# Performance work log

Hardware: AMD Instinct MI355X
Metric: run time of the kernel (lower is better)

## Reference

```python
import jax, jax.numpy as jnp
import numpy as np
import math

CH = 256
GROUPS = max(min(CH // 4, 32), 1)  # default_num_groups -> 32
EPS = 1e-5


def group_norm(x, gamma, beta):
    # x: [B, C, H, W]
    B, C, H, W = x.shape
    xg = x.reshape(B, GROUPS, C // GROUPS, H, W)
    mu = jnp.mean(xg, axis=(2, 3, 4), keepdims=True)
    var = jnp.var(xg, axis=(2, 3, 4), keepdims=True)
    xn = ((xg - mu) * jax.lax.rsqrt(var + EPS)).reshape(B, C, H, W)
    return xn * gamma[None, :, None, None] + beta[None, :, None, None]


def conv1x1(x, w, b):
    # x: [B, C_in, H, W]; w: [C_out, C_in]; b: [C_out]
    return jnp.einsum('oc,bchw->bohw', w, x) + b[None, :, None, None]


def xavier(key, shape, gain):
    fan_in, fan_out = shape[1], shape[0]
    limit = gain * math.sqrt(6.0 / (fan_in + fan_out))
    return jax.random.uniform(key, shape, jnp.float32, -limit, limit)


def setup_inputs() -> dict:
    key = jax.random.key(0)
    ks = jax.random.split(key, 6)
    x = jax.random.normal(ks[0], (32, CH, 32, 32), jnp.float32)
    gamma = jnp.ones((CH,), jnp.float32)
    beta = jnp.zeros((CH,), jnp.float32)
    g = math.sqrt(0.1)  # init_scale=0.1 for q,k,v
    wq = xavier(ks[1], (CH, CH), g)
    wk = xavier(ks[2], (CH, CH), g)
    wv = xavier(ks[3], (CH, CH), g)
    # w_h uses init_scale=0.0 -> zeros in original; use small nonzero so output is exercised
    wh = xavier(ks[4], (CH, CH), 0.1)
    bq = jnp.zeros((CH,), jnp.float32)
    bk = jnp.zeros((CH,), jnp.float32)
    bv = jnp.zeros((CH,), jnp.float32)
    bh = jnp.zeros((CH,), jnp.float32)
    return dict(x=x, gamma=gamma, beta=beta, wq=wq, bq=bq, wk=wk, bk=bk,
                wv=wv, bv=bv, wh=wh, bh=bh)


def reference(x, gamma, beta, wq, bq, wk, bk, wv, bv, wh, bh):
    B, C, H, W = x.shape
    N = H * W
    h = group_norm(x, gamma, beta)
    q = conv1x1(h, wq, bq).reshape(B, C, N)
    k = conv1x1(h, wk, bk).reshape(B, C, N)
    v = conv1x1(h, wv, bv).reshape(B, C, N)
    # full attention over spatial tokens: scores [B, N, N]
    scores = jnp.einsum('bcn,bcm->bnm', q, k) / math.sqrt(C)
    attn = jax.nn.softmax(scores, axis=-1)
    h = jnp.einsum('bnm,bcm->bcn', attn, v).reshape(B, C, H, W)
    h = conv1x1(h, wh, bh)
    return x + h  # skip_rescale=False
```

## Files before the change

kernel.cpp:

```cpp
#include <hip/hip_runtime.h>

typedef __bf16 bf16_t;
typedef __bf16 bf16x8 __attribute__((ext_vector_type(8)));
typedef __bf16 bf16x4 __attribute__((ext_vector_type(4)));
typedef float f32x4 __attribute__((ext_vector_type(4)));
typedef float f32x16 __attribute__((ext_vector_type(16)));
typedef long longx2 __attribute__((ext_vector_type(2)));

static constexpr int kC = 256;
static constexpr int kN = 1024;
static constexpr int kB = 32;

__device__ __forceinline__ void gload_lds16(const void* g, void* l) {
  __builtin_amdgcn_global_load_lds(
      (const __attribute__((address_space(1))) unsigned int*)g,
      (__attribute__((address_space(3))) unsigned int*)l, 16, 0, 0);
}

__device__ __forceinline__ unsigned cvt_pk_bf16(float a, float b) {
  unsigned r;
  asm("v_cvt_pk_bf16_f32 %0, %1, %2" : "=v"(r) : "v"(a), "v"(b));
  return r;
}

__device__ __forceinline__ unsigned pk_fp8x4(float a, float b, float c, float d) {
  unsigned r;
  asm("v_cvt_pk_fp8_f32 %0, %1, %2" : "=v"(r) : "v"(a), "v"(b));
  asm("v_cvt_pk_fp8_f32 %0, %1, %2 op_sel:[0,0,1]" : "+v"(r) : "v"(c), "v"(d));
  return r;
}

__device__ __forceinline__ void pl32swap(unsigned& a, unsigned& b) {
  asm("v_permlane32_swap_b32 %0, %1" : "+v"(a), "+v"(b));
}

__device__ __forceinline__ float cross_half_sum(float rs) {
  unsigned a = __builtin_bit_cast(unsigned, rs), b = a;
  pl32swap(a, b);
  return __builtin_bit_cast(float, a) + __builtin_bit_cast(float, b);
}

__global__ __launch_bounds__(256) void gn_castw_k(const float* __restrict__ x,
                                                  const float* __restrict__ gamma,
                                                  const float* __restrict__ beta,
                                                  bf16_t* __restrict__ hn,
                                                  const float* __restrict__ wq,
                                                  const float* __restrict__ wk,
                                                  const float* __restrict__ wv,
                                                  const float* __restrict__ wh,
                                                  bf16_t* __restrict__ wb) {
  __shared__ float xs[8 * 1040];
  __shared__ float red[8];
  __shared__ float stat[2];
  int t = threadIdx.x;
  if (blockIdx.x >= 1024) {
    int i = (blockIdx.x - 1024) * 256 + t;
    wb[i] = (bf16_t)wq[i];
    wb[i + 65536] = (bf16_t)wk[i];
    wb[i + 131072] = (bf16_t)wv[i];
    wb[i + 196608] = (bf16_t)wh[i];
    return;
  }
  int bg = blockIdx.x;
  int b = bg >> 5, g = bg & 31;
  const float* base = x + (size_t)bg * 8192;
  float s = 0.f, q = 0.f;
#pragma unroll
  for (int i = 0; i < 8; ++i) {
    float4 v = *(const float4*)(base + i * 1024 + t * 4);
    *(float4*)(xs + i * 1040 + t * 4) = v;
    s += v.x + v.y + v.z + v.w;
    q += v.x * v.x + v.y * v.y + v.z * v.z + v.w * v.w;
  }
#pragma unroll
  for (int o = 32; o; o >>= 1) { s += __shfl_down(s, o); q += __shfl_down(q, o); }
  int w = t >> 6;
  if ((t & 63) == 0) { red[w] = s; red[4 + w] = q; }
  __syncthreads();
  if (t == 0) {
    float S = red[0] + red[1] + red[2] + red[3];
    float Q = red[4] + red[5] + red[6] + red[7];
    float mean = S * (1.f / 8192.f);
    float var = Q * (1.f / 8192.f) - mean * mean;
    stat[0] = mean;
    stat[1] = rsqrtf(var + 1e-5f);
  }
  __syncthreads();
  float mean = stat[0], rstd = stat[1];
  float gmb[8], btb[8];
#pragma unroll
  for (int j = 0; j < 8; ++j) { gmb[j] = gamma[g * 8 + j]; btb[j] = beta[g * 8 + j]; }
  bf16_t* hb = hn + (size_t)b * (kN * kC) + g * 8;
#pragma unroll
  for (int i = 0; i < 4; ++i) {
    int n = i * 256 + t;
    bf16x8 o;
#pragma unroll
    for (int j = 0; j < 8; ++j)
      o[j] = (bf16_t)((xs[j * 1040 + n] - mean) * rstd * gmb[j] + btb[j]);
    *(bf16x8*)(hb + (size_t)n * kC) = o;
  }
}

__global__ __launch_bounds__(256, 2) void fattn_k(const char* __restrict__ QT,
                                                  const char* __restrict__ KT,
                                                  const bf16_t* __restrict__ VV,
                                                  bf16_t* __restrict__ OT) {
  __shared__ char smem[49152];
  char* lKc = smem;
  bf16_t* lV = (bf16_t*)(smem + 16384);
  int t = threadIdx.x;
  int wid = t >> 6, lane = t & 63;
  int l31 = lane & 31, hi = lane >> 5;
  int qg = wid & 1, h = wid >> 1;
  int bid = blockIdx.x;
  int b = ((bid & 7) << 2) | ((bid >> 3) & 3);
  int qt = bid >> 5;
  const char* Qb = QT + (size_t)b * (kN * kC);
  int q0 = qt * 64 + qg * 32;
  constexpr float kSc = 0.0625f * 1.44269504f;

  long qf[16];
#pragma unroll
  for (int jj = 0; jj < 8; ++jj) {
    longx2 qp = *(const longx2*)(Qb + (size_t)(q0 + l31) * kC + hi * 128 + jj * 16);
    qf[2 * jj] = qp[0];
    qf[2 * jj + 1] = qp[1];
  }

  unsigned koff2[8];
#pragma unroll
  for (int jj = 0; jj < 8; ++jj)
    koff2[jj] = l31 * 256 + (((hi * 8 + jj) ^ (l31 & 15)) << 4);
  unsigned voff[8];
#pragma unroll
  for (int gs = 0; gs < 2; ++gs)
#pragma unroll
    for (int ct = 0; ct < 4; ++ct) {
      int c = h * 128 + ct * 32 + l31;
      voff[gs * 4 + ct] = c * 32 + (((gs * 2 + hi) ^ ((c >> 1) & 3)) << 3);
    }

  unsigned koffg[2], voffg[4];
#pragma unroll
  for (int i = 0; i < 2; ++i) {
    int ck = i * 256 + t;
    int row = ck >> 4, s = ck & 15;
    koffg[i] = row * 256 + ((s ^ (row & 15)) << 4);
  }
#pragma unroll
  for (int i = 0; i < 4; ++i) {
    int cv = i * 256 + t;
    int c = cv >> 2, s = cv & 3;
    voffg[i] = c * 1024 + ((s ^ ((c >> 1) & 3)) << 3);
  }
  const char* kSrc = KT + (size_t)b * (kN * kC);
  const bf16_t* vSrc = VV + (size_t)b * (kC * kN);
  char* kd0 = lKc + t * 16;
  bf16_t* vd0 = lV + t * 8;

  f32x16 acc[4] = {};
  float lsum = 0.f;

  auto STAGE = [&](int buf) {
#pragma unroll
    for (int i = 0; i < 2; ++i)
      gload_lds16(kSrc + koffg[i], kd0 + buf * 8192 + i * 4096);
#pragma unroll
    for (int i = 0; i < 4; ++i)
      gload_lds16(vSrc + voffg[i], vd0 + buf * 8192 + i * 2048);
    kSrc += 8192;
    vSrc += 32;
  };

  auto COMPUTE = [&](int buf) {
    const char* bK = lKc + buf * 8192;
    const bf16_t* bV = lV + buf * 8192;
    f32x16 sa = {}, sb = {};
    __builtin_amdgcn_s_setprio(1);
#pragma unroll
    for (int jj = 0; jj < 4; ++jj) {
      longx2 ka = *(const longx2*)(bK + koff2[jj]);
      longx2 kb = *(const longx2*)(bK + koff2[jj + 4]);
      sa = __builtin_amdgcn_mfma_f32_32x32x16_fp8_fp8(ka[0], qf[2 * jj], sa, 0, 0, 0);
      sb = __builtin_amdgcn_mfma_f32_32x32x16_fp8_fp8(kb[0], qf[8 + 2 * jj], sb, 0, 0, 0);
      sa = __builtin_amdgcn_mfma_f32_32x32x16_fp8_fp8(ka[1], qf[2 * jj + 1], sa, 0, 0, 0);
      sb = __builtin_amdgcn_mfma_f32_32x32x16_fp8_fp8(kb[1], qf[9 + 2 * jj], sb, 0, 0, 0);
    }
    __builtin_amdgcn_s_setprio(0);
    float rs = 0.f;
    float e0, e1, e2, e3, e4, e5, e6, e7;
    e0 = exp2f((sa[0] + sb[0]) * kSc); e1 = exp2f((sa[1] + sb[1]) * kSc);
    e2 = exp2f((sa[2] + sb[2]) * kSc); e3 = exp2f((sa[3] + sb[3]) * kSc);
    e4 = exp2f((sa[4] + sb[4]) * kSc); e5 = exp2f((sa[5] + sb[5]) * kSc);
    e6 = exp2f((sa[6] + sb[6]) * kSc); e7 = exp2f((sa[7] + sb[7]) * kSc);
    rs += e0 + e1 + e2 + e3 + e4 + e5 + e6 + e7;
    unsigned A0 = cvt_pk_bf16(e0, e1), A1 = cvt_pk_bf16(e2, e3);
    unsigned B0 = cvt_pk_bf16(e4, e5), B1 = cvt_pk_bf16(e6, e7);
    pl32swap(A0, B0);
    pl32swap(A1, B1);
    uint4 u0 = make_uint4(A0, A1, B0, B1);
    bf16x8 pa0 = __builtin_bit_cast(bf16x8, u0);
    __builtin_amdgcn_s_setprio(1);
#pragma unroll
    for (int ct = 0; ct < 4; ++ct) {
      bf16x8 vf = *(const bf16x8*)(bV + voff[ct]);
      acc[ct] = __builtin_amdgcn_mfma_f32_32x32x16_bf16(pa0, vf, acc[ct], 0, 0, 0);
    }
    __builtin_amdgcn_s_setprio(0);
    e0 = exp2f((sa[8] + sb[8]) * kSc);   e1 = exp2f((sa[9] + sb[9]) * kSc);
    e2 = exp2f((sa[10] + sb[10]) * kSc); e3 = exp2f((sa[11] + sb[11]) * kSc);
    e4 = exp2f((sa[12] + sb[12]) * kSc); e5 = exp2f((sa[13] + sb[13]) * kSc);
    e6 = exp2f((sa[14] + sb[14]) * kSc); e7 = exp2f((sa[15] + sb[15]) * kSc);
    rs += e0 + e1 + e2 + e3 + e4 + e5 + e6 + e7;
    unsigned C0 = cvt_pk_bf16(e0, e1), C1 = cvt_pk_bf16(e2, e3);
    unsigned D0 = cvt_pk_bf16(e4, e5), D1 = cvt_pk_bf16(e6, e7);
    pl32swap(C0, D0);
    pl32swap(C1, D1);
    uint4 u1 = make_uint4(C0, C1, D0, D1);
    bf16x8 pa1 = __builtin_bit_cast(bf16x8, u1);
    __builtin_amdgcn_s_setprio(1);
#pragma unroll
    for (int ct = 0; ct < 4; ++ct) {
      bf16x8 vf = *(const bf16x8*)(bV + voff[4 + ct]);
      acc[ct] = __builtin_amdgcn_mfma_f32_32x32x16_bf16(pa1, vf, acc[ct], 0, 0, 0);
    }
    __builtin_amdgcn_s_setprio(0);
    lsum += rs;
  };

  STAGE(0);
  for (int kt = 0; kt < 32; ++kt) {
    if (kt < 31) {
      STAGE((kt + 1) & 1);
      asm volatile("s_waitcnt vmcnt(6)" ::: "memory");
    } else {
      asm volatile("s_waitcnt vmcnt(0)" ::: "memory");
    }
    __builtin_amdgcn_s_barrier();
    COMPUTE(kt & 1);
    __builtin_amdgcn_s_barrier();
  }

  lsum = cross_half_sum(lsum);
  float inv = 1.f / lsum;
  float invR[16];
#pragma unroll
  for (int r = 0; r < 16; ++r)
    invR[r] = __shfl(inv, (r & 3) + 8 * (r >> 2) + 4 * hi);
  bf16_t* Ob = OT + (size_t)b * (kN * kC);
#pragma unroll
  for (int ct = 0; ct < 4; ++ct)
#pragma unroll
    for (int r = 0; r < 16; ++r) {
      int qr = (r & 3) + 8 * (r >> 2) + 4 * hi;
      Ob[(size_t)(q0 + qr) * kC + h * 128 + ct * 32 + l31] =
          (bf16_t)(acc[ct][r] * invR[r]);
    }
}

__global__ __launch_bounds__(256) void qkv_gemm_k(const bf16_t* __restrict__ W,
                                                  const bf16_t* __restrict__ HNall,
                                                  char* __restrict__ QTo,
                                                  char* __restrict__ KTo,
                                                  bf16_t* __restrict__ VVo,
                                                  const float* __restrict__ bq,
                                                  const float* __restrict__ bk,
                                                  const float* __restrict__ bv) {
  __shared__ bf16_t lA[2][128 * 64];
  __shared__ bf16_t lB[2][128 * 64];
  int bid = blockIdx.x;
  int b = bid / 48;
  int rem = bid - b * 48;
  int tmi = rem >> 3, tni = rem & 7;
  const bf16_t* Ab = W + (size_t)tmi * 128 * 256;
  const bf16_t* Bb = HNall + (size_t)b * (kN * kC) + (size_t)tni * 128 * 256;
  int t = threadIdx.x;
  int wid = t >> 6, l = t & 63;
  int wm = wid >> 1, wn = wid & 1;
  int lr = l & 15, lk = l >> 4;
  unsigned goff[4];
#pragma unroll
  for (int i = 0; i < 4; ++i) {
    int ci = i * 256 + t;
    int row = ci >> 3, s = ci & 7;
    goff[i] = row * 256 + ((s ^ (row & 7)) << 3);
  }
  unsigned aoff[8], boff[8];
#pragma unroll
  for (int kk = 0; kk < 2; ++kk)
#pragma unroll
    for (int f = 0; f < 4; ++f) {
      int ra = wm * 64 + f * 16 + lr;
      int rb2 = wn * 64 + f * 16 + lr;
      int ch = kk * 4 + lk;
      aoff[kk * 4 + f] = ra * 64 + ((ch ^ (ra & 7)) << 3);
      boff[kk * 4 + f] = rb2 * 64 + ((ch ^ (rb2 & 7)) << 3);
    }
  f32x4 acc[4][4] = {};
  auto STAGE = [&](int buf, int k0) {
#pragma unroll
    for (int i = 0; i < 4; ++i) {
      gload_lds16(Ab + k0 + goff[i], &lA[buf][t * 8 + i * 2048]);
      gload_lds16(Bb + k0 + goff[i], &lB[buf][t * 8 + i * 2048]);
    }
  };
  STAGE(0, 0);
  for (int kt = 0; kt < 4; ++kt) {
    if (kt < 3) {
      STAGE((kt + 1) & 1, (kt + 1) * 64);
      asm volatile("s_waitcnt vmcnt(8)" ::: "memory");
    } else {
      asm volatile("s_waitcnt vmcnt(0)" ::: "memory");
    }
    __builtin_amdgcn_s_barrier();
    const bf16_t* cA = lA[kt & 1];
    const bf16_t* cB = lB[kt & 1];
#pragma unroll
    for (int kk = 0; kk < 2; ++kk) {
      bf16x8 af[4], bfr[4];
#pragma unroll
      for (int f = 0; f < 4; ++f) {
        af[f] = *(const bf16x8*)(cA + aoff[kk * 4 + f]);
        bfr[f] = *(const bf16x8*)(cB + boff[kk * 4 + f]);
      }
#pragma unroll
      for (int mf = 0; mf < 4; ++mf)
#pragma unroll
        for (int nf = 0; nf < 4; ++nf)
          acc[mf][nf] = __builtin_amdgcn_mfma_f32_16x16x32_bf16(af[mf], bfr[nf],
                                                                acc[mf][nf], 0, 0, 0);
    }
    __builtin_amdgcn_s_barrier();
  }
  int seg = tmi >> 1;
  int rb = (tmi & 1) * 128 + wm * 64;
  int cb = tni * 128 + wn * 64;
  if (seg < 2) {
    char* D = (seg ? KTo : QTo) + (size_t)b * (kN * kC);
    const float* bias = seg ? bk : bq;
#pragma unroll
    for (int mf = 0; mf < 4; ++mf)
#pragma unroll
      for (int nf = 0; nf < 4; ++nf) {
        int r0 = rb + mf * 16 + lk * 4;
        int c = cb + nf * 16 + lr;
        unsigned u = pk_fp8x4(acc[mf][nf][0] + bias[r0], acc[mf][nf][1] + bias[r0 + 1],
                              acc[mf][nf][2] + bias[r0 + 2], acc[mf][nf][3] + bias[r0 + 3]);
        int np = ((r0 >> 3) & 1) * 128 + (r0 >> 4) * 8 + (r0 & 7);
        *(unsigned*)(D + (size_t)c * kC + np) = u;
      }
  } else {
    bf16_t* D = VVo + (size_t)b * (kC * kN);
#pragma unroll
    for (int mf = 0; mf < 4; ++mf)
#pragma unroll
      for (int nf = 0; nf < 4; ++nf) {
        int r0 = rb + mf * 16 + lk * 4;
        int c = cb + nf * 16 + lr;
#pragma unroll
        for (int i = 0; i < 4; ++i)
          D[(size_t)(r0 + i) * kN + c] = (bf16_t)(acc[mf][nf][i] + bv[r0 + i]);
      }
  }
}

__global__ __launch_bounds__(256) void out_gemm_k(const bf16_t* __restrict__ A,
                                                  const bf16_t* __restrict__ BT,
                                                  float* __restrict__ Dst,
                                                  const float* __restrict__ bias,
                                                  const float* __restrict__ resid) {
  __shared__ bf16_t lA[2][128 * 64];
  __shared__ bf16_t lB[2][128 * 64];
  int bid = blockIdx.x;
  int b = bid >> 4;
  int rem = bid & 15;
  int tmi = rem >> 1, tni = rem & 1;
  const bf16_t* Ab = A + (size_t)b * (kN * kC) + (size_t)tmi * 128 * 256;
  const bf16_t* Bb = BT + (size_t)tni * 128 * 256;
  int t = threadIdx.x;
  int wid = t >> 6, l = t & 63;
  int wm = wid >> 1, wn = wid & 1;
  int lr = l & 15, lk = l >> 4;
  unsigned goff[4];
#pragma unroll
  for (int i = 0; i < 4; ++i) {
    int ci = i * 256 + t;
    int row = ci >> 3, s = ci & 7;
    goff[i] = row * 256 + ((s ^ (row & 7)) << 3);
  }
  unsigned aoff[8], boff[8];
#pragma unroll
  for (int kk = 0; kk < 2; ++kk)
#pragma unroll
    for (int f = 0; f < 4; ++f) {
      int ra = wm * 64 + f * 16 + lr;
      int rb2 = wn * 64 + f * 16 + lr;
      int ch = kk * 4 + lk;
      aoff[kk * 4 + f] = ra * 64 + ((ch ^ (ra & 7)) << 3);
      boff[kk * 4 + f] = rb2 * 64 + ((ch ^ (rb2 & 7)) << 3);
    }
  f32x4 acc[4][4] = {};
  auto STAGE = [&](int buf, int k0) {
#pragma unroll
    for (int i = 0; i < 4; ++i) {
      gload_lds16(Ab + k0 + goff[i], &lA[buf][t * 8 + i * 2048]);
      gload_lds16(Bb + k0 + goff[i], &lB[buf][t * 8 + i * 2048]);
    }
  };
  STAGE(0, 0);
  for (int kt = 0; kt < 4; ++kt) {
    if (kt < 3) {
      STAGE((kt + 1) & 1, (kt + 1) * 64);
      asm volatile("s_waitcnt vmcnt(8)" ::: "memory");
    } else {
      asm volatile("s_waitcnt vmcnt(0)" ::: "memory");
    }
    __builtin_amdgcn_s_barrier();
    const bf16_t* cA = lA[kt & 1];
    const bf16_t* cB = lB[kt & 1];
#pragma unroll
    for (int kk = 0; kk < 2; ++kk) {
      bf16x8 af[4], bfr[4];
#pragma unroll
      for (int f = 0; f < 4; ++f) {
        af[f] = *(const bf16x8*)(cA + aoff[kk * 4 + f]);
        bfr[f] = *(const bf16x8*)(cB + boff[kk * 4 + f]);
      }
#pragma unroll
      for (int mf = 0; mf < 4; ++mf)
#pragma unroll
        for (int nf = 0; nf < 4; ++nf)
          acc[mf][nf] = __builtin_amdgcn_mfma_f32_16x16x32_bf16(af[mf], bfr[nf],
                                                                acc[mf][nf], 0, 0, 0);
    }
    __builtin_amdgcn_s_barrier();
  }
  int rb = tmi * 128 + wm * 64;
  int cb = tni * 128 + wn * 64;
  float* D = Dst + (size_t)b * (kC * kN);
  const float* R = resid + (size_t)b * (kC * kN);
#pragma unroll
  for (int mf = 0; mf < 4; ++mf)
#pragma unroll
    for (int nf = 0; nf < 4; ++nf) {
      int r0 = rb + mf * 16 + lk * 4;
      int c = cb + nf * 16 + lr;
      float4 rv = *(const float4*)(R + (size_t)c * kN + r0);
      float bc = bias[c];
      float4 o2 = make_float4(acc[mf][nf][0] + rv.x + bc, acc[mf][nf][1] + rv.y + bc,
                              acc[mf][nf][2] + rv.z + bc, acc[mf][nf][3] + rv.w + bc);
      *(float4*)(D + (size_t)c * kN + r0) = o2;
    }
}

extern "C" void kernel_launch(void* const* d_in, const int* in_sizes, int n_in,
                              void* d_out, int out_size, void* d_ws, size_t ws_size,
                              hipStream_t stream) {
  (void)in_sizes; (void)n_in; (void)out_size; (void)ws_size;
  const float* x = (const float*)d_in[0];
  const float* gamma = (const float*)d_in[1];
  const float* beta = (const float*)d_in[2];
  const float* wq = (const float*)d_in[3];
  const float* bq = (const float*)d_in[4];
  const float* wk = (const float*)d_in[5];
  const float* bk = (const float*)d_in[6];
  const float* wv = (const float*)d_in[7];
  const float* bv = (const float*)d_in[8];
  const float* wh = (const float*)d_in[9];
  const float* bh = (const float*)d_in[10];
  float* out = (float*)d_out;

  char* ws = (char*)d_ws;
  bf16_t* HN = (bf16_t*)(ws);
  char* QT = ws + 16777216;
  char* KT = ws + 25165824;
  bf16_t* VV = (bf16_t*)(ws + 33554432);
  bf16_t* WB = (bf16_t*)(ws + 50331648);

  gn_castw_k<<<kB * 32 + 256, 256, 0, stream>>>(x, gamma, beta, HN, wq, wk, wv, wh, WB);
  qkv_gemm_k<<<kB * 48, 256, 0, stream>>>(WB, HN, QT, KT, VV, bq, bk, bv);
  fattn_k<<<512, 256, 0, stream>>>(QT, KT, VV, HN);
  out_gemm_k<<<kB * 16, 256, 0, stream>>>(HN, WB + 196608, out, bh, x);
}
```

Measured before the change: 120.0 us.

## Use FP8 for V and P in attention and split keys across wave pairs

The V projection is now stored as FP8 in a swizzled layout, and the P·V product uses FP8 MFMA on P probabilities packed to FP8 instead of BF16. The attention tile grows to 64 keys per iteration. Each wave pair splits the key dimension, sharing P through LDS with an extra barrier per iteration, and the row sums are combined through LDS at the end. This halves V bandwidth and MFMA cost for P·V, but loses accuracy from FP8 probabilities and values, uses more LDS per block (which may lower occupancy), and adds synchronization.

```diff
diff --git a/kernel.cpp b/kernel.cpp
--- a/kernel.cpp
+++ b/kernel.cpp
@@ -6,6 +6,7 @@
 typedef float f32x4 __attribute__((ext_vector_type(4)));
 typedef float f32x16 __attribute__((ext_vector_type(16)));
 typedef long longx2 __attribute__((ext_vector_type(2)));
+typedef unsigned uintx2 __attribute__((ext_vector_type(2)));
 
 static constexpr int kC = 256;
 static constexpr int kN = 1024;
@@ -15,12 +16,6 @@
   __builtin_amdgcn_global_load_lds(
       (const __attribute__((address_space(1))) unsigned int*)g,
       (__attribute__((address_space(3))) unsigned int*)l, 16, 0, 0);
-}
-
-__device__ __forceinline__ unsigned cvt_pk_bf16(float a, float b) {
-  unsigned r;
-  asm("v_cvt_pk_bf16_f32 %0, %1, %2" : "=v"(r) : "v"(a), "v"(b));
-  return r;
 }
 
 __device__ __forceinline__ unsigned pk_fp8x4(float a, float b, float c, float d) {
@@ -104,11 +99,13 @@
 
 __global__ __launch_bounds__(256, 2) void fattn_k(const char* __restrict__ QT,
                                                   const char* __restrict__ KT,
-                                                  const bf16_t* __restrict__ VV,
+                                                  const char* __restrict__ VV,
                                                   bf16_t* __restrict__ OT) {
-  __shared__ char smem[49152];
+  __shared__ char smem[70656];
   char* lKc = smem;
-  bf16_t* lV = (bf16_t*)(smem + 16384);
+  char* lVc = smem + 32768;
+  char* pb = smem + 65536;
+  float* exls = (float*)(smem + 69632);
   int t = threadIdx.x;
   int wid = t >> 6, lane = t & 63;
   int l31 = lane & 31, hi = lane >> 5;
@@ -131,119 +128,112 @@
   unsigned koff2[8];
 #pragma unroll
   for (int jj = 0; jj < 8; ++jj)
-    koff2[jj] = l31 * 256 + (((hi * 8 + jj) ^ (l31 & 15)) << 4);
-  unsigned voff[8];
-#pragma unroll
-  for (int gs = 0; gs < 2; ++gs)
+    koff2[jj] = (h * 32 + l31) * 256 + (((hi * 8 + jj) ^ (l31 & 15)) << 4);
+  unsigned voff2[8];
+#pragma unroll
+  for (int sp = 0; sp < 2; ++sp)
 #pragma unroll
     for (int ct = 0; ct < 4; ++ct) {
       int c = h * 128 + ct * 32 + l31;
-      voff[gs * 4 + ct] = c * 32 + (((gs * 2 + hi) ^ ((c >> 1) & 3)) << 3);
-    }
-
-  unsigned koffg[2], voffg[4];
-#pragma unroll
-  for (int i = 0; i < 2; ++i) {
+      voff2[sp * 4 + ct] = c * 64 + ((sp ^ ((c >> 1) & 1)) << 5) + hi * 16;
+    }
+
+  unsigned koffg[4], voffg[4];
+#pragma unroll
+  for (int i = 0; i < 4; ++i) {
     int ck = i * 256 + t;
     int row = ck >> 4, s = ck & 15;
     koffg[i] = row * 256 + ((s ^ (row & 15)) << 4);
-  }
-#pragma unroll
-  for (int i = 0; i < 4; ++i) {
     int cv = i * 256 + t;
-    int c = cv >> 2, s = cv & 3;
-    voffg[i] = c * 1024 + ((s ^ ((c >> 1) & 3)) << 3);
+    voffg[i] = (cv >> 2) * 1024 + ((cv & 3) << 4);
   }
   const char* kSrc = KT + (size_t)b * (kN * kC);
-  const bf16_t* vSrc = VV + (size_t)b * (kC * kN);
+  const char* vSrc = VV + (size_t)b * (kC * kN);
   char* kd0 = lKc + t * 16;
-  bf16_t* vd0 = lV + t * 8;
+  char* vd0 = lVc + t * 16;
 
   f32x16 acc[4] = {};
   float lsum = 0.f;
 
   auto STAGE = [&](int buf) {
 #pragma unroll
-    for (int i = 0; i < 2; ++i)
-      gload_lds16(kSrc + koffg[i], kd0 + buf * 8192 + i * 4096);
-#pragma unroll
     for (int i = 0; i < 4; ++i)
-      gload_lds16(vSrc + voffg[i], vd0 + buf * 8192 + i * 2048);
-    kSrc += 8192;
-    vSrc += 32;
+      gload_lds16(kSrc + koffg[i], kd0 + buf * 16384 + i * 4096);
+#pragma unroll
+    for (int i = 0; i < 4; ++i)
+      gload_lds16(vSrc + voffg[i], vd0 + buf * 16384 + i * 4096);
+    kSrc += 16384;
+    vSrc += 64;
   };
 
-  auto COMPUTE = [&](int buf) {
-    const char* bK = lKc + buf * 8192;
-    const bf16_t* bV = lV + buf * 8192;
-    f32x16 sa = {}, sb = {};
+  STAGE(0);
+  for (int kt = 0; kt < 16; ++kt) {
+    if (kt < 15) {
+      STAGE((kt + 1) & 1);
+      asm volatile("s_waitcnt vmcnt(8)" ::: "memory");
+    } else {
+      asm volatile("s_waitcnt vmcnt(0)" ::: "memory");
+    }
+    __builtin_amdgcn_s_barrier();
+    const char* bK = lKc + (kt & 1) * 16384;
+    const char* bV = lVc + (kt & 1) * 16384;
+    f32x16 sa = {};
     __builtin_amdgcn_s_setprio(1);
 #pragma unroll
-    for (int jj = 0; jj < 4; ++jj) {
+    for (int jj = 0; jj < 8; ++jj) {
       longx2 ka = *(const longx2*)(bK + koff2[jj]);
-      longx2 kb = *(const longx2*)(bK + koff2[jj + 4]);
       sa = __builtin_amdgcn_mfma_f32_32x32x16_fp8_fp8(ka[0], qf[2 * jj], sa, 0, 0, 0);
-      sb = __builtin_amdgcn_mfma_f32_32x32x16_fp8_fp8(kb[0], qf[8 + 2 * jj], sb, 0, 0, 0);
       sa = __builtin_amdgcn_mfma_f32_32x32x16_fp8_fp8(ka[1], qf[2 * jj + 1], sa, 0, 0, 0);
-      sb = __builtin_amdgcn_mfma_f32_32x32x16_fp8_fp8(kb[1], qf[9 + 2 * jj], sb, 0, 0, 0);
     }
     __builtin_amdgcn_s_setprio(0);
     float rs = 0.f;
-    float e0, e1, e2, e3, e4, e5, e6, e7;
-    e0 = exp2f((sa[0] + sb[0]) * kSc); e1 = exp2f((sa[1] + sb[1]) * kSc);
-    e2 = exp2f((sa[2] + sb[2]) * kSc); e3 = exp2f((sa[3] + sb[3]) * kSc);
-    e4 = exp2f((sa[4] + sb[4]) * kSc); e5 = exp2f((sa[5] + sb[5]) * kSc);
-    e6 = exp2f((sa[6] + sb[6]) * kSc); e7 = exp2f((sa[7] + sb[7]) * kSc);
+    float e0 = exp2f(sa[0] * kSc), e1 = exp2f(sa[1] * kSc);
+    float e2 = exp2f(sa[2] * kSc), e3 = exp2f(sa[3] * kSc);
+    float e4 = exp2f(sa[4] * kSc), e5 = exp2f(sa[5] * kSc);
+    float e6 = exp2f(sa[6] * kSc), e7 = exp2f(sa[7] * kSc);
     rs += e0 + e1 + e2 + e3 + e4 + e5 + e6 + e7;
-    unsigned A0 = cvt_pk_bf16(e0, e1), A1 = cvt_pk_bf16(e2, e3);
-    unsigned B0 = cvt_pk_bf16(e4, e5), B1 = cvt_pk_bf16(e6, e7);
-    pl32swap(A0, B0);
-    pl32swap(A1, B1);
-    uint4 u0 = make_uint4(A0, A1, B0, B1);
-    bf16x8 pa0 = __builtin_bit_cast(bf16x8, u0);
+    unsigned G0 = pk_fp8x4(e0, e1, e2, e3), G1 = pk_fp8x4(e4, e5, e6, e7);
+    pl32swap(G0, G1);
+    e0 = exp2f(sa[8] * kSc);  e1 = exp2f(sa[9] * kSc);
+    e2 = exp2f(sa[10] * kSc); e3 = exp2f(sa[11] * kSc);
+    e4 = exp2f(sa[12] * kSc); e5 = exp2f(sa[13] * kSc);
+    e6 = exp2f(sa[14] * kSc); e7 = exp2f(sa[15] * kSc);
+    rs += e0 + e1 + e2 + e3 + e4 + e5 + e6 + e7;
+    lsum += rs;
+    unsigned G2 = pk_fp8x4(e0, e1, e2, e3), G3 = pk_fp8x4(e4, e5, e6, e7);
+    pl32swap(G2, G3);
+    *(uint4*)(pb + wid * 1024 + lane * 16) = make_uint4(G0, G1, G2, G3);
+    asm volatile("s_waitcnt lgkmcnt(0)" ::: "memory");
+    __builtin_amdgcn_s_barrier();
+    uint4 po = *(const uint4*)(pb + (wid ^ 2) * 1024 + lane * 16);
+    long own0 = __builtin_bit_cast(long, uintx2{G0, G1});
+    long own1 = __builtin_bit_cast(long, uintx2{G2, G3});
+    long pr0 = __builtin_bit_cast(long, uintx2{po.x, po.y});
+    long pr1 = __builtin_bit_cast(long, uintx2{po.z, po.w});
+    long s0 = h ? pr0 : own0, s1 = h ? pr1 : own1;
+    long s2 = h ? own0 : pr0, s3 = h ? own1 : pr1;
     __builtin_amdgcn_s_setprio(1);
 #pragma unroll
     for (int ct = 0; ct < 4; ++ct) {
-      bf16x8 vf = *(const bf16x8*)(bV + voff[ct]);
-      acc[ct] = __builtin_amdgcn_mfma_f32_32x32x16_bf16(pa0, vf, acc[ct], 0, 0, 0);
+      longx2 vv = *(const longx2*)(bV + voff2[ct]);
+      acc[ct] = __builtin_amdgcn_mfma_f32_32x32x16_fp8_fp8(s0, vv[0], acc[ct], 0, 0, 0);
+      acc[ct] = __builtin_amdgcn_mfma_f32_32x32x16_fp8_fp8(s1, vv[1], acc[ct], 0, 0, 0);
+    }
+#pragma unroll
+    for (int ct = 0; ct < 4; ++ct) {
+      longx2 vv = *(const longx2*)(bV + voff2[4 + ct]);
+      acc[ct] = __builtin_amdgcn_mfma_f32_32x32x16_fp8_fp8(s2, vv[0], acc[ct], 0, 0, 0);
+      acc[ct] = __builtin_amdgcn_mfma_f32_32x32x16_fp8_fp8(s3, vv[1], acc[ct], 0, 0, 0);
     }
     __builtin_amdgcn_s_setprio(0);
-    e0 = exp2f((sa[8] + sb[8]) * kSc);   e1 = exp2f((sa[9] + sb[9]) * kSc);
-    e2 = exp2f((sa[10] + sb[10]) * kSc); e3 = exp2f((sa[11] + sb[11]) * kSc);
-    e4 = exp2f((sa[12] + sb[12]) * kSc); e5 = exp2f((sa[13] + sb[13]) * kSc);
-    e6 = exp2f((sa[14] + sb[14]) * kSc); e7 = exp2f((sa[15] + sb[15]) * kSc);
-    rs += e0 + e1 + e2 + e3 + e4 + e5 + e6 + e7;
-    unsigned C0 = cvt_pk_bf16(e0, e1), C1 = cvt_pk_bf16(e2, e3);
-    unsigned D0 = cvt_pk_bf16(e4, e5), D1 = cvt_pk_bf16(e6, e7);
-    pl32swap(C0, D0);
-    pl32swap(C1, D1);
-    uint4 u1 = make_uint4(C0, C1, D0, D1);
-    bf16x8 pa1 = __builtin_bit_cast(bf16x8, u1);
-    __builtin_amdgcn_s_setprio(1);
-#pragma unroll
-    for (int ct = 0; ct < 4; ++ct) {
-      bf16x8 vf = *(const bf16x8*)(bV + voff[4 + ct]);
-      acc[ct] = __builtin_amdgcn_mfma_f32_32x32x16_bf16(pa1, vf, acc[ct], 0, 0, 0);
-    }
-    __builtin_amdgcn_s_setprio(0);
-    lsum += rs;
-  };
-
-  STAGE(0);
-  for (int kt = 0; kt < 32; ++kt) {
-    if (kt < 31) {
-      STAGE((kt + 1) & 1);
-      asm volatile("s_waitcnt vmcnt(6)" ::: "memory");
-    } else {
-      asm volatile("s_waitcnt vmcnt(0)" ::: "memory");
-    }
-    __builtin_amdgcn_s_barrier();
-    COMPUTE(kt & 1);
-    __builtin_amdgcn_s_barrier();
-  }
-
-  lsum = cross_half_sum(lsum);
-  float inv = 1.f / lsum;
+    __builtin_amdgcn_s_barrier();
+  }
+
+  float ls = cross_half_sum(lsum);
+  exls[wid * 64 + lane] = ls;
+  __syncthreads();
+  ls += exls[(wid ^ 2) * 64 + lane];
+  float inv = 1.f / ls;
   float invR[16];
 #pragma unroll
   for (int r = 0; r < 16; ++r)
@@ -263,7 +253,7 @@
                                                   const bf16_t* __restrict__ HNall,
                                                   char* __restrict__ QTo,
                                                   char* __restrict__ KTo,
-                                                  bf16_t* __restrict__ VVo,
+                                                  char* __restrict__ VVo,
                                                   const float* __restrict__ bq,
                                                   const float* __restrict__ bk,
                                                   const float* __restrict__ bv) {
@@ -351,16 +341,24 @@
         *(unsigned*)(D + (size_t)c * kC + np) = u;
       }
   } else {
-    bf16_t* D = VVo + (size_t)b * (kC * kN);
+    char* D = VVo + (size_t)b * (kC * kN);
 #pragma unroll
     for (int mf = 0; mf < 4; ++mf)
 #pragma unroll
       for (int nf = 0; nf < 4; ++nf) {
         int r0 = rb + mf * 16 + lk * 4;
         int c = cb + nf * 16 + lr;
-#pragma unroll
-        for (int i = 0; i < 4; ++i)
-          D[(size_t)(r0 + i) * kN + c] = (bf16_t)(acc[mf][nf][i] + bv[r0 + i]);
+        unsigned u = pk_fp8x4(acc[mf][nf][0] + bv[r0], acc[mf][nf][1] + bv[r0 + 1],
+                              acc[mf][nf][2] + bv[r0 + 2], acc[mf][nf][3] + bv[r0 + 3]);
+        int kv = c & 63, tile = c >> 6;
+        int sp = kv >> 5;
+        int base = tile * 64 + ((kv >> 3) & 1) * 16 + ((kv >> 4) & 1) * 8 + (kv & 7);
+#pragma unroll
+        for (int i = 0; i < 4; ++i) {
+          int ch = r0 + i;
+          int pos = base + ((sp ^ ((ch >> 1) & 1)) << 5);
+          D[(size_t)ch * kN + pos] = (char)(u >> (8 * i));
+        }
       }
   }
 }
@@ -475,7 +473,7 @@
   bf16_t* HN = (bf16_t*)(ws);
   char* QT = ws + 16777216;
   char* KT = ws + 25165824;
-  bf16_t* VV = (bf16_t*)(ws + 33554432);
+  char* VV = ws + 33554432;
   bf16_t* WB = (bf16_t*)(ws + 50331648);
 
   gn_castw_k<<<kB * 32 + 256, 256, 0, stream>>>(x, gamma, beta, HN, wq, wk, wv, wh, WB);
```

New measurement: 102.2 us (median of 2 runs). 14.8% less time.
